# Performance work log

Measured on AMD Instinct MI355X. Metric: run time of the kernel, lower is better.

Reference implementation:

```python
import jax, jax.numpy as jnp
import numpy as np

B, T, C, H, FF = 4, 2048, 768, 12, 3072
D = C // H
EPS = 1e-5


def setup_inputs() -> dict:
    key = jax.random.key(0)
    ks = jax.random.split(key, 8)
    s = 0.02
    return {
        "x": jax.random.normal(ks[0], (B, T, C), jnp.float32),
        "ln1_w": jnp.ones((C,), jnp.float32),
        "ln1_b": jnp.zeros((C,), jnp.float32),
        "qkv_w": jax.random.normal(ks[1], (C, 3 * C), jnp.float32) * s,
        "qkv_b": jnp.zeros((3 * C,), jnp.float32),
        "out_w": jax.random.normal(ks[2], (C, C), jnp.float32) * s,
        "out_b": jnp.zeros((C,), jnp.float32),
        "ln2_w": jnp.ones((C,), jnp.float32),
        "ln2_b": jnp.zeros((C,), jnp.float32),
        "ff1_w": jax.random.normal(ks[3], (C, FF), jnp.float32) * s,
        "ff1_b": jnp.zeros((FF,), jnp.float32),
        "ff2_w": jax.random.normal(ks[4], (FF, C), jnp.float32) * s,
        "ff2_b": jnp.zeros((C,), jnp.float32),
    }


def _layernorm(x, w, b):
    m = jnp.mean(x, axis=-1, keepdims=True)
    v = jnp.mean(jnp.square(x - m), axis=-1, keepdims=True)
    return (x - m) * jax.lax.rsqrt(v + EPS) * w + b


def reference(x, ln1_w, ln1_b, qkv_w, qkv_b, out_w, out_b,
              ln2_w, ln2_b, ff1_w, ff1_b, ff2_w, ff2_b):
    # --- attention sublayer ---
    h = _layernorm(x, ln1_w, ln1_b)
    qkv = h @ qkv_w + qkv_b                      # [B,T,3C]
    q, k, v = jnp.split(qkv, 3, axis=-1)
    q = q.reshape(B, T, H, D)
    k = k.reshape(B, T, H, D)
    v = v.reshape(B, T, H, D)
    scores = jnp.einsum('bthd,bshd->bhts', q, k) / np.sqrt(D).astype(np.float32)
    causal = jnp.tril(jnp.ones((T, T), bool))    # [T,T]
    scores = jnp.where(causal[None, None], scores, -jnp.inf)
    attn = jax.nn.softmax(scores, axis=-1)       # [B,H,T,T]
    o = jnp.einsum('bhts,bshd->bthd', attn, v).reshape(B, T, C)
    x = x + o @ out_w + out_b
    # --- FFN sublayer ---
    h2 = _layernorm(x, ln2_w, ln2_b)
    x = x + jax.nn.relu(h2 @ ff1_w + ff1_b) @ ff2_w + ff2_b
    return x
```

## Files before the change

### kernel.cpp

```cpp
#include <hip/hip_runtime.h>
#include <hip/hip_bf16.h>
#include <cstdint>
#include <cstddef>

#define B_ 4
#define T_ 2048
#define C_ 768
#define H_ 12
#define D_ 64
#define FF_ 3072

typedef __attribute__((ext_vector_type(4))) float f32x4;
typedef __attribute__((ext_vector_type(8))) short s16x8;
typedef __attribute__((ext_vector_type(4))) short s16x4;

static __device__ __forceinline__ short f2bf(float f) {
  union { float fv; unsigned u; } v; v.fv = f;
  unsigned r = v.u + 0x7FFFu + ((v.u >> 16) & 1u);
  return (short)(r >> 16);
}

static __device__ __forceinline__ unsigned pkbf2(float a, float b) {
  __hip_bfloat162 h = __float22bfloat162_rn(make_float2(a, b));
  union { __hip_bfloat162 h2; unsigned u; } v; v.h2 = h;
  return v.u;
}

__global__ __launch_bounds__(256) void wconv(const float* __restrict__ in,
                                             short* __restrict__ out,
                                             int K, int N) {
  __shared__ float tile[32][33];
  int tk = blockIdx.x * 32, tn = blockIdx.y * 32;
  int lx = threadIdx.x & 31, ly = threadIdx.x >> 5;
#pragma unroll
  for (int i = 0; i < 4; ++i)
    tile[ly + i * 8][lx] = in[(size_t)(tk + ly + i * 8) * N + tn + lx];
  __syncthreads();
#pragma unroll
  for (int i = 0; i < 4; ++i)
    out[(size_t)(tn + ly + i * 8) * K + tk + lx] = f2bf(tile[lx][ly + i * 8]);
}

__global__ __launch_bounds__(256) void ln_kernel(const float* __restrict__ x,
                                                 const float* __restrict__ w,
                                                 const float* __restrict__ b,
                                                 short* __restrict__ out) {
  int row = blockIdx.x, tid = threadIdx.x;
  const float* xr = x + (size_t)row * 768;
  float v0 = xr[tid], v1 = xr[tid + 256], v2 = xr[tid + 512];
  float s = v0 + v1 + v2;
#pragma unroll
  for (int o = 32; o > 0; o >>= 1) s += __shfl_down(s, o);
  __shared__ float r1[4], r2[4];
  if ((tid & 63) == 0) r1[tid >> 6] = s;
  __syncthreads();
  float mean = (r1[0] + r1[1] + r1[2] + r1[3]) * (1.f / 768.f);
  float d0 = v0 - mean, d1 = v1 - mean, d2 = v2 - mean;
  float q = d0 * d0 + d1 * d1 + d2 * d2;
#pragma unroll
  for (int o = 32; o > 0; o >>= 1) q += __shfl_down(q, o);
  if ((tid & 63) == 0) r2[tid >> 6] = q;
  __syncthreads();
  float var = (r2[0] + r2[1] + r2[2] + r2[3]) * (1.f / 768.f);
  float rstd = rsqrtf(var + 1e-5f);
  short* orow = out + (size_t)row * 768;
  orow[tid]       = f2bf(d0 * rstd * w[tid]       + b[tid]);
  orow[tid + 256] = f2bf(d1 * rstd * w[tid + 256] + b[tid + 256]);
  orow[tid + 512] = f2bf(d2 * rstd * w[tid + 512] + b[tid + 512]);
}

template <int MODE>
__global__ __launch_bounds__(256) void gemm_bt(
    const short* __restrict__ A, const short* __restrict__ Bt,
    const float* __restrict__ bias, const float* __restrict__ res,
    void* __restrict__ out,
    short* __restrict__ dq, short* __restrict__ dk, short* __restrict__ dv,
    int M, int N, int K) {
  __shared__ short As[2][128 * 32];
  __shared__ short Bs[2][128 * 32];
  int tid = threadIdx.x;
  int lane = tid & 63;
  int wm = tid >> 7;
  int wn = (tid >> 6) & 1;
  const short* Ab = A + (size_t)blockIdx.x * 128 * K;
  const short* Bb = Bt + (size_t)blockIdx.y * 128 * K;
  f32x4 acc[4][4] = {};
  int i15 = lane & 15, g8 = (lane >> 4) << 3;
  int nk = K >> 6;
  for (int kt = 0; kt < nk; ++kt) {
    int kof = kt << 6;
#pragma unroll
    for (int i = 0; i < 4; ++i) {
      int s = tid + i * 256;
      int pan = s >> 9, sp = s & 511;
      int row = sp >> 2, kk = ((sp & 3) << 3) + (pan << 5);
      __builtin_amdgcn_global_load_lds(
          (const __attribute__((address_space(1))) unsigned*)(Ab + (size_t)row * K + kof + kk),
          (__attribute__((address_space(3))) unsigned*)(&As[pan][sp * 8]), 16, 0, 0);
      __builtin_amdgcn_global_load_lds(
          (const __attribute__((address_space(1))) unsigned*)(Bb + (size_t)row * K + kof + kk),
          (__attribute__((address_space(3))) unsigned*)(&Bs[pan][sp * 8]), 16, 0, 0);
    }
    __syncthreads();
#pragma unroll
    for (int h = 0; h < 2; ++h) {
      s16x8 af[4], bfr[4];
#pragma unroll
      for (int m = 0; m < 4; ++m)
        af[m] = *(const s16x8*)(&As[h][(wm * 64 + m * 16 + i15) * 32 + g8]);
#pragma unroll
      for (int n = 0; n < 4; ++n)
        bfr[n] = *(const s16x8*)(&Bs[h][(wn * 64 + n * 16 + i15) * 32 + g8]);
#pragma unroll
      for (int m = 0; m < 4; ++m)
#pragma unroll
        for (int n = 0; n < 4; ++n)
          acc[m][n] = __builtin_amdgcn_mfma_f32_16x16x32_bf16(af[m], bfr[n], acc[m][n], 0, 0, 0);
    }
    __syncthreads();
  }
  int row0 = blockIdx.x * 128 + wm * 64;
  int col0 = blockIdx.y * 128 + wn * 64;
  int g4 = (lane >> 4) << 2;
#pragma unroll
  for (int m = 0; m < 4; ++m) {
#pragma unroll
    for (int n = 0; n < 4; ++n) {
      int col = col0 + n * 16 + i15;
      float bv = bias[col];
      float v4[4];
#pragma unroll
      for (int r = 0; r < 4; ++r) v4[r] = acc[m][n][r] + bv;
      int rbase = row0 + m * 16 + g4;
      if constexpr (MODE == 0) {
        int sect = col / 768;
        int wi = col - sect * 768;
        int hh = wi >> 6, dd = wi & 63;
        int bb = rbase >> 11, tt = rbase & 2047;
        if (sect == 2) {
          s16x4 o4;
#pragma unroll
          for (int r = 0; r < 4; ++r) o4[r] = f2bf(v4[r]);
          *(s16x4*)(dv + ((size_t)(bb * H_ + hh) * D_ + dd) * T_ + tt) = o4;
        } else {
          short* dst = (sect == 0 ? dq : dk) + ((size_t)(bb * H_ + hh) * T_ + tt) * D_ + dd;
          float sc = sect == 0 ? 0.18033688f : 1.f;
#pragma unroll
          for (int r = 0; r < 4; ++r) dst[(size_t)r * D_] = f2bf(v4[r] * sc);
        }
      } else {
#pragma unroll
        for (int r = 0; r < 4; ++r)
          ((short*)out)[(size_t)(rbase + r) * N + col] = f2bf(v4[r] > 0.f ? v4[r] : 0.f);
      }
    }
  }
}

__global__ __launch_bounds__(128, 3) void gemm64_res(
    const short* __restrict__ A, const short* __restrict__ Bt,
    const float* __restrict__ bias, const float* __restrict__ res,
    float* __restrict__ out, int M, int N, int K) {
  __shared__ short As[2][64 * 32];
  __shared__ short Bs[2][128 * 32];
  int tid = threadIdx.x;
  int lane = tid & 63;
  int wn = tid >> 6;
  const short* Ab = A + (size_t)blockIdx.x * 64 * K;
  const short* Bb = Bt + (size_t)blockIdx.y * 128 * K;
  f32x4 acc[4][4] = {};
  int i15 = lane & 15, g8 = (lane >> 4) << 3;
  int nk = K >> 6;
  for (int kt = 0; kt < nk; ++kt) {
    int kof = kt << 6;
#pragma unroll
    for (int i = 0; i < 4; ++i) {
      int c = tid + i * 128;
      int pan = c >> 8, sp = c & 255;
      int row = sp >> 2, kk = ((sp & 3) << 3) + (pan << 5);
      __builtin_amdgcn_global_load_lds(
          (const __attribute__((address_space(1))) unsigned*)(Ab + (size_t)row * K + kof + kk),
          (__attribute__((address_space(3))) unsigned*)(&As[pan][sp * 8]), 16, 0, 0);
    }
#pragma unroll
    for (int i = 0; i < 8; ++i) {
      int c = tid + i * 128;
      int pan = c >> 9, sp = c & 511;
      int row = sp >> 2, kk = ((sp & 3) << 3) + (pan << 5);
      __builtin_amdgcn_global_load_lds(
          (const __attribute__((address_space(1))) unsigned*)(Bb + (size_t)row * K + kof + kk),
          (__attribute__((address_space(3))) unsigned*)(&Bs[pan][sp * 8]), 16, 0, 0);
    }
    __syncthreads();
#pragma unroll
    for (int h = 0; h < 2; ++h) {
      s16x8 af[4], bfr[4];
#pragma unroll
      for (int m = 0; m < 4; ++m)
        af[m] = *(const s16x8*)(&As[h][(m * 16 + i15) * 32 + g8]);
#pragma unroll
      for (int n = 0; n < 4; ++n)
        bfr[n] = *(const s16x8*)(&Bs[h][(wn * 64 + n * 16 + i15) * 32 + g8]);
#pragma unroll
      for (int m = 0; m < 4; ++m)
#pragma unroll
        for (int n = 0; n < 4; ++n)
          acc[m][n] = __builtin_amdgcn_mfma_f32_16x16x32_bf16(af[m], bfr[n], acc[m][n], 0, 0, 0);
    }
    __syncthreads();
  }
  int row0 = blockIdx.x * 64;
  int col0 = blockIdx.y * 128 + wn * 64;
  int g4 = (lane >> 4) << 2;
#pragma unroll
  for (int m = 0; m < 4; ++m) {
#pragma unroll
    for (int n = 0; n < 4; ++n) {
      int col = col0 + n * 16 + i15;
      float bv = bias[col];
      int rbase = row0 + m * 16 + g4;
#pragma unroll
      for (int r = 0; r < 4; ++r)
        out[(size_t)(rbase + r) * N + col] =
            acc[m][n][r] + bv + res[(size_t)(rbase + r) * N + col];
    }
  }
}

__global__ __launch_bounds__(256) void attn_kernel(const short* __restrict__ Qb,
                                                   const short* __restrict__ Kb,
                                                   const short* __restrict__ VTb,
                                                   short* __restrict__ Ob) {
  __shared__ short Ks[2][4096];
  __shared__ short Vs[2][4096];
  int i = blockIdx.x;
  int c = i & 7, j = i >> 3;
  int qb = 31 - (j & 31);
  int gy = j >> 5;
  int bh = c + (gy << 3);
  int bb = bh / H_, hh = bh - bb * H_;
  int tid = threadIdx.x, lane = tid & 63, wv = tid >> 6;
  int q0 = qb << 6;
  int nt = qb + 1;
  const short* Qp = Qb + (size_t)bh * T_ * D_;
  const short* Kp = Kb + (size_t)bh * T_ * D_;
  const short* Vp = VTb + (size_t)bh * D_ * T_;
  int i15 = lane & 15, g = lane >> 4, g8 = g << 3;
  int keyA0 = ((i15 >> 2) << 3) + (i15 & 3);
  int keyB0 = keyA0 + 4;
  int fA = (keyA0 & 7) ^ ((keyA0 & 8) >> 1);
  int fB = (keyB0 & 7) ^ ((keyB0 & 8) >> 1);
  int fV = (i15 & 7) ^ ((i15 & 8) >> 1);
  int oA[2], oB[2], oV[2];
#pragma unroll
  for (int h = 0; h < 2; ++h) {
    oA[h] = keyA0 * 64 + (((h * 4 + g) ^ fA) << 3);
    oB[h] = keyB0 * 64 + (((h * 4 + g) ^ fB) << 3);
    oV[h] = i15 * 64 + (((h * 4 + g) ^ fV) << 3);
  }
  int qrow = q0 + wv * 16 + i15;
  s16x8 qf0 = *(const s16x8*)(Qp + (size_t)qrow * D_ + g8);
  s16x8 qf1 = *(const s16x8*)(Qp + (size_t)qrow * D_ + 32 + g8);
  f32x4 oacc[4] = {};
  float lsum = 0.f;

  auto stage = [&](int buf, int t) {
    int k0 = t << 6;
#pragma unroll
    for (int qq = 0; qq < 2; ++qq) {
      int m = tid + qq * 256;
      int r = m >> 3, cd = m & 7;
      int cs = cd ^ ((r & 7) ^ ((r & 8) >> 1));
      __builtin_amdgcn_global_load_lds(
          (const __attribute__((address_space(1))) unsigned*)(Kp + (size_t)(k0 + r) * D_ + (cs << 3)),
          (__attribute__((address_space(3))) unsigned*)(&Ks[buf][m * 8]), 16, 0, 0);
      __builtin_amdgcn_global_load_lds(
          (const __attribute__((address_space(1))) unsigned*)(Vp + (size_t)r * T_ + k0 + (cs << 3)),
          (__attribute__((address_space(3))) unsigned*)(&Vs[buf][m * 8]), 16, 0, 0);
    }
  };

  stage(0, 0);
  __syncthreads();
  int cur = 0;
#pragma unroll 1
  for (int t = 0; t < nt; ++t) {
    if (t + 1 < nt) stage(cur ^ 1, t + 1);
    const short* KB = &Ks[cur][0];
    const short* VB = &Vs[cur][0];
    bool diag = (t == nt - 1);
    int k0 = t << 6;
#pragma unroll
    for (int ks = 0; ks < 2; ++ks) {
      if (!(ks == 1 && diag && wv < 2)) {
        s16x8 ka0 = *(const s16x8*)(KB + (ks << 11) + oA[0]);
        s16x8 ka1 = *(const s16x8*)(KB + (ks << 11) + oA[1]);
        s16x8 kb0 = *(const s16x8*)(KB + (ks << 11) + oB[0]);
        s16x8 kb1 = *(const s16x8*)(KB + (ks << 11) + oB[1]);
        f32x4 sA = {}, sB = {};
        __builtin_amdgcn_s_setprio(1);
        sA = __builtin_amdgcn_mfma_f32_16x16x32_bf16(ka0, qf0, sA, 0, 0, 0);
        sA = __builtin_amdgcn_mfma_f32_16x16x32_bf16(ka1, qf1, sA, 0, 0, 0);
        sB = __builtin_amdgcn_mfma_f32_16x16x32_bf16(kb0, qf0, sB, 0, 0, 0);
        sB = __builtin_amdgcn_mfma_f32_16x16x32_bf16(kb1, qf1, sB, 0, 0, 0);
        __builtin_amdgcn_s_setprio(0);
        int kb = k0 + (ks << 5) + g8;
        float sa[8];
        bool needmask = diag && ((wv < 2) == (ks == 0));
        if (needmask) {
#pragma unroll
          for (int r = 0; r < 4; ++r) {
            sa[r]     = (kb + r     <= qrow) ? sA[r] : -1e30f;
            sa[4 + r] = (kb + 4 + r <= qrow) ? sB[r] : -1e30f;
          }
        } else {
#pragma unroll
          for (int r = 0; r < 4; ++r) { sa[r] = sA[r]; sa[4 + r] = sB[r]; }
        }
        float p[8];
        float ps = 0.f;
#pragma unroll
        for (int r = 0; r < 8; ++r) {
          p[r] = exp2f(sa[r]);
          ps += p[r];
        }
        lsum += ps;
        union { unsigned u[4]; s16x8 v; } pf;
        pf.u[0] = pkbf2(p[0], p[1]);
        pf.u[1] = pkbf2(p[2], p[3]);
        pf.u[2] = pkbf2(p[4], p[5]);
        pf.u[3] = pkbf2(p[6], p[7]);
        s16x8 vf0 = *(const s16x8*)(VB + 0    + oV[ks]);
        s16x8 vf1 = *(const s16x8*)(VB + 1024 + oV[ks]);
        s16x8 vf2 = *(const s16x8*)(VB + 2048 + oV[ks]);
        s16x8 vf3 = *(const s16x8*)(VB + 3072 + oV[ks]);
        __builtin_amdgcn_s_setprio(1);
        oacc[0] = __builtin_amdgcn_mfma_f32_16x16x32_bf16(vf0, pf.v, oacc[0], 0, 0, 0);
        oacc[1] = __builtin_amdgcn_mfma_f32_16x16x32_bf16(vf1, pf.v, oacc[1], 0, 0, 0);
        oacc[2] = __builtin_amdgcn_mfma_f32_16x16x32_bf16(vf2, pf.v, oacc[2], 0, 0, 0);
        oacc[3] = __builtin_amdgcn_mfma_f32_16x16x32_bf16(vf3, pf.v, oacc[3], 0, 0, 0);
        __builtin_amdgcn_s_setprio(0);
      }
    }
    __syncthreads();
    cur ^= 1;
  }
  float l = lsum;
  l += __shfl_xor(l, 16);
  l += __shfl_xor(l, 32);
  float inv = 1.f / l;
  short* op = Ob + ((size_t)(bb * T_ + qrow)) * C_ + hh * D_ + (g << 2);
#pragma unroll
  for (int mt = 0; mt < 4; ++mt) {
    s16x4 o4;
#pragma unroll
    for (int r = 0; r < 4; ++r) o4[r] = f2bf(oacc[mt][r] * inv);
    *(s16x4*)(op + mt * 16) = o4;
  }
}

extern "C" void kernel_launch(void* const* d_in, const int* in_sizes, int n_in,
                              void* d_out, int out_size, void* d_ws, size_t ws_size,
                              hipStream_t stream) {
  const float* x     = (const float*)d_in[0];
  const float* ln1_w = (const float*)d_in[1];
  const float* ln1_b = (const float*)d_in[2];
  const float* qkv_w = (const float*)d_in[3];
  const float* qkv_b = (const float*)d_in[4];
  const float* out_w = (const float*)d_in[5];
  const float* out_b = (const float*)d_in[6];
  const float* ln2_w = (const float*)d_in[7];
  const float* ln2_b = (const float*)d_in[8];
  const float* ff1_w = (const float*)d_in[9];
  const float* ff1_b = (const float*)d_in[10];
  const float* ff2_w = (const float*)d_in[11];
  const float* ff2_b = (const float*)d_in[12];

  char* ws = (char*)d_ws;
  short* Wqkv = (short*)(ws + 0);
  short* Wout = (short*)(ws + 3538944);
  short* Wff1 = (short*)(ws + 4718592);
  short* Wff2 = (short*)(ws + 9437184);
  short* Hbuf = (short*)(ws + 14155776);
  short* Qb   = (short*)(ws + 26738688);
  short* Kb   = Qb + 6291456;
  short* VT   = Kb + 6291456;
  short* Ob   = VT + 6291456;
  short* FFH  = Qb;
  float* xout = (float*)d_out;

  wconv<<<dim3(24, 72), 256, 0, stream>>>(qkv_w, Wqkv, 768, 2304);
  wconv<<<dim3(24, 24), 256, 0, stream>>>(out_w, Wout, 768, 768);
  wconv<<<dim3(24, 96), 256, 0, stream>>>(ff1_w, Wff1, 768, 3072);
  wconv<<<dim3(96, 24), 256, 0, stream>>>(ff2_w, Wff2, 3072, 768);

  ln_kernel<<<8192, 256, 0, stream>>>(x, ln1_w, ln1_b, Hbuf);
  gemm_bt<0><<<dim3(64, 18), 256, 0, stream>>>(Hbuf, Wqkv, qkv_b, nullptr, nullptr,
                                               Qb, Kb, VT, 8192, 2304, 768);
  attn_kernel<<<1536, 256, 0, stream>>>(Qb, Kb, VT, Ob);
  gemm64_res<<<dim3(128, 6), 128, 0, stream>>>(Ob, Wout, out_b, x, xout, 8192, 768, 768);
  ln_kernel<<<8192, 256, 0, stream>>>(xout, ln2_w, ln2_b, Hbuf);
  gemm_bt<2><<<dim3(64, 24), 256, 0, stream>>>(Hbuf, Wff1, ff1_b, nullptr, FFH,
                                               nullptr, nullptr, nullptr, 8192, 3072, 768);
  gemm64_res<<<dim3(128, 6), 128, 0, stream>>>(FFH, Wff2, ff2_b, xout, xout, 8192, 768, 3072);
}
```

Measured before the change: 288.4 us.

## Pair causal attention query blocks per workgroup to balance work

Each attention workgroup now processes two query blocks, p and 31-p, back to back, so every block runs exactly 33 key tiles instead of 1 to 32. The grid is halved to 768 blocks and the K/V staging pipeline continues across the switch between the two query blocks. This removes the causal load imbalance and the tail effect, at the cost of fewer workgroups for latency hiding and an extra finalize and Q reload midway through.

```diff
diff --git a/kernel.cpp b/kernel.cpp
--- a/kernel.cpp
+++ b/kernel.cpp
@@ -235,13 +235,10 @@
   __shared__ short Vs[2][4096];
   int i = blockIdx.x;
   int c = i & 7, j = i >> 3;
-  int qb = 31 - (j & 31);
-  int gy = j >> 5;
+  int p = j & 15, gy = j >> 4;
   int bh = c + (gy << 3);
   int bb = bh / H_, hh = bh - bb * H_;
   int tid = threadIdx.x, lane = tid & 63, wv = tid >> 6;
-  int q0 = qb << 6;
-  int nt = qb + 1;
   const short* Qp = Qb + (size_t)bh * T_ * D_;
   const short* Kp = Kb + (size_t)bh * T_ * D_;
   const short* Vp = VTb + (size_t)bh * D_ * T_;
@@ -258,12 +255,17 @@
     oB[h] = keyB0 * 64 + (((h * 4 + g) ^ fB) << 3);
     oV[h] = i15 * 64 + (((h * 4 + g) ^ fV) << 3);
   }
-  int qrow = q0 + wv * 16 + i15;
-  s16x8 qf0 = *(const s16x8*)(Qp + (size_t)qrow * D_ + g8);
-  s16x8 qf1 = *(const s16x8*)(Qp + (size_t)qrow * D_ + 32 + g8);
+  int n0 = p + 1;
+  s16x8 qf0, qf1;
   f32x4 oacc[4] = {};
   float lsum = 0.f;
-
+  int qrow = 0;
+
+  auto loadQ = [&](int qb) {
+    qrow = (qb << 6) + wv * 16 + i15;
+    qf0 = *(const s16x8*)(Qp + (size_t)qrow * D_ + g8);
+    qf1 = *(const s16x8*)(Qp + (size_t)qrow * D_ + 32 + g8);
+  };
   auto stage = [&](int buf, int t) {
     int k0 = t << 6;
 #pragma unroll
@@ -279,17 +281,37 @@
           (__attribute__((address_space(3))) unsigned*)(&Vs[buf][m * 8]), 16, 0, 0);
     }
   };
-
+  auto finalize = [&]() {
+    float l = lsum;
+    l += __shfl_xor(l, 16);
+    l += __shfl_xor(l, 32);
+    float inv = 1.f / l;
+    short* op = Ob + ((size_t)(bb * T_ + qrow)) * C_ + hh * D_ + (g << 2);
+#pragma unroll
+    for (int mt = 0; mt < 4; ++mt) {
+      s16x4 o4;
+#pragma unroll
+      for (int r = 0; r < 4; ++r) o4[r] = f2bf(oacc[mt][r] * inv);
+      *(s16x4*)(op + mt * 16) = o4;
+    }
+  };
+
+  loadQ(p);
   stage(0, 0);
   __syncthreads();
   int cur = 0;
 #pragma unroll 1
-  for (int t = 0; t < nt; ++t) {
-    if (t + 1 < nt) stage(cur ^ 1, t + 1);
+  for (int gt = 0; gt < 33; ++gt) {
+    if (gt + 1 < 33) {
+      int nkt = (gt + 1 < n0) ? (gt + 1) : (gt + 1 - n0);
+      stage(cur ^ 1, nkt);
+    }
+    int kt = (gt < n0) ? gt : gt - n0;
+    int nt = (gt < n0) ? n0 : 32 - p;
+    bool diag = (kt == nt - 1);
+    int k0 = kt << 6;
     const short* KB = &Ks[cur][0];
     const short* VB = &Vs[cur][0];
-    bool diag = (t == nt - 1);
-    int k0 = t << 6;
 #pragma unroll
     for (int ks = 0; ks < 2; ++ks) {
       if (!(ks == 1 && diag && wv < 2)) {
@@ -317,19 +339,19 @@
 #pragma unroll
           for (int r = 0; r < 4; ++r) { sa[r] = sA[r]; sa[4 + r] = sB[r]; }
         }
-        float p[8];
+        float pv[8];
         float ps = 0.f;
 #pragma unroll
         for (int r = 0; r < 8; ++r) {
-          p[r] = exp2f(sa[r]);
-          ps += p[r];
+          pv[r] = exp2f(sa[r]);
+          ps += pv[r];
         }
         lsum += ps;
         union { unsigned u[4]; s16x8 v; } pf;
-        pf.u[0] = pkbf2(p[0], p[1]);
-        pf.u[1] = pkbf2(p[2], p[3]);
-        pf.u[2] = pkbf2(p[4], p[5]);
-        pf.u[3] = pkbf2(p[6], p[7]);
+        pf.u[0] = pkbf2(pv[0], pv[1]);
+        pf.u[1] = pkbf2(pv[2], pv[3]);
+        pf.u[2] = pkbf2(pv[4], pv[5]);
+        pf.u[3] = pkbf2(pv[6], pv[7]);
         s16x8 vf0 = *(const s16x8*)(VB + 0    + oV[ks]);
         s16x8 vf1 = *(const s16x8*)(VB + 1024 + oV[ks]);
         s16x8 vf2 = *(const s16x8*)(VB + 2048 + oV[ks]);
@@ -342,21 +364,17 @@
         __builtin_amdgcn_s_setprio(0);
       }
     }
+    if (gt == n0 - 1) {
+      finalize();
+      loadQ(31 - p);
+#pragma unroll
+      for (int mt = 0; mt < 4; ++mt) oacc[mt] = f32x4{0.f, 0.f, 0.f, 0.f};
+      lsum = 0.f;
+    }
     __syncthreads();
     cur ^= 1;
   }
-  float l = lsum;
-  l += __shfl_xor(l, 16);
-  l += __shfl_xor(l, 32);
-  float inv = 1.f / l;
-  short* op = Ob + ((size_t)(bb * T_ + qrow)) * C_ + hh * D_ + (g << 2);
-#pragma unroll
-  for (int mt = 0; mt < 4; ++mt) {
-    s16x4 o4;
-#pragma unroll
-    for (int r = 0; r < 4; ++r) o4[r] = f2bf(oacc[mt][r] * inv);
-    *(s16x4*)(op + mt * 16) = o4;
-  }
+  finalize();
 }
 
 extern "C" void kernel_launch(void* const* d_in, const int* in_sizes, int n_in,
@@ -397,7 +415,7 @@
   ln_kernel<<<8192, 256, 0, stream>>>(x, ln1_w, ln1_b, Hbuf);
   gemm_bt<0><<<dim3(64, 18), 256, 0, stream>>>(Hbuf, Wqkv, qkv_b, nullptr, nullptr,
                                                Qb, Kb, VT, 8192, 2304, 768);
-  attn_kernel<<<1536, 256, 0, stream>>>(Qb, Kb, VT, Ob);
+  attn_kernel<<<768, 256, 0, stream>>>(Qb, Kb, VT, Ob);
   gemm64_res<<<dim3(128, 6), 128, 0, stream>>>(Ob, Wout, out_b, x, xout, 8192, 768, 768);
   ln_kernel<<<8192, 256, 0, stream>>>(xout, ln2_w, ln2_b, Hbuf);
   gemm_bt<2><<<dim3(64, 24), 256, 0, stream>>>(Hbuf, Wff1, ff1_b, nullptr, FFH,
```

Measured after the change: 280.4 us. 1.03x faster.
